# Performance work log

Hardware: AMD Instinct MI355X
Metric: run time of the kernel (lower is better)

## Reference

```python
import jax, jax.numpy as jnp
import numpy as np

N = 10000      # nodes
E = 80000      # edges
D = 128        # d_model
H = 8          # num_heads
DH = 128       # d_head
DFF = 512      # d_ff
CLAMP = 5.0
EPS = 1e-5


def setup_inputs() -> dict:
    key = jax.random.key(0)
    ks = jax.random.split(key, 10)
    s = 0.05
    return {
        "feat": jax.random.normal(ks[0], (N, D), jnp.float32),
        "src": jax.random.randint(ks[1], (E,), 0, N),
        "dst": jax.random.randint(ks[2], (E,), 0, N),
        # projections stored as (in, out); x @ W == torch Linear(bias=False)
        "Wq": jax.random.normal(ks[3], (D, H * DH), jnp.float32) * s,
        "Wk": jax.random.normal(ks[4], (D, H * DH), jnp.float32) * s,
        "Wv": jax.random.normal(ks[5], (D, H * DH), jnp.float32) * s,
        "Wo": jax.random.normal(ks[6], (H * DH, D), jnp.float32) * s,
        "g1": jnp.ones((D,), jnp.float32),
        "b1": jnp.zeros((D,), jnp.float32),
        "W1": jax.random.normal(ks[7], (D, DFF), jnp.float32) * s,
        "bf1": jnp.zeros((DFF,), jnp.float32),
        "W2": jax.random.normal(ks[8], (DFF, D), jnp.float32) * s,
        "bf2": jnp.zeros((D,), jnp.float32),
        "g2": jnp.ones((D,), jnp.float32),
        "b2": jnp.zeros((D,), jnp.float32),
    }


def _layer_norm(x, g, b):
    mu = x.mean(-1, keepdims=True)
    xc = x - mu
    var = (xc * xc).mean(-1, keepdims=True)
    return xc * jax.lax.rsqrt(var + EPS) * g + b


def reference(feat, src, dst, Wq, Wk, Wv, Wo, g1, b1, W1, bf1, W2, bf2, g2, b2):
    h_src = feat[src]                              # (E, D) gather
    h_dst = feat[dst]                              # (E, D)
    q = (h_dst @ Wq).reshape(E, H, DH)             # query from destination node
    k = (h_src @ Wk).reshape(E, H, DH)
    v = (h_src @ Wv).reshape(E, H, DH)
    # per-edge logits: QK dot per head, scale, clamp
    u = jnp.clip((q * k).sum(-1) / np.sqrt(DH), -CLAMP, CLAMP)  # (E, H)
    # edge_softmax over incoming edges of each destination node
    m = jax.ops.segment_max(u, dst, num_segments=N)             # (N, H)
    ex = jnp.exp(u - m[dst])
    den = jax.ops.segment_sum(ex, dst, num_segments=N)          # (N, H)
    a = ex / den[dst]                                           # (E, H)
    # weighted V, segment-sum to destination nodes
    agg = jax.ops.segment_sum(a[..., None] * v, dst, num_segments=N)  # (N, H, DH)
    uh = _layer_norm(feat + agg.reshape(N, H * DH) @ Wo, g1, b1)
    ffn = jax.nn.relu(uh @ W1 + bf1) @ W2 + bf2
    return _layer_norm(uh + ffn, g2, b2)
```

## Files before the change

### kernel.cpp

```cpp
#include <hip/hip_runtime.h>

typedef unsigned int uint;
typedef unsigned short ushort;
typedef __attribute__((ext_vector_type(8))) short short8;
typedef __attribute__((ext_vector_type(4))) float f32x4;

#define DEV static __device__ __forceinline__

DEV float bf_lo(uint v) { return __uint_as_float(v << 16); }
DEV float bf_hi(uint v) { return __uint_as_float(v & 0xffff0000u); }
DEV ushort f2bf(float f) {
    uint u = __float_as_uint(f);
    u += 0x7fffu + ((u >> 16) & 1u);
    return (ushort)(u >> 16);
}
DEV void stC(float* p, float v) { *p = v; }
DEV void stC(ushort* p, float v) { *p = f2bf(v); }

#define DPPADD(v, ctrl) \
    ((v) + __int_as_float(__builtin_amdgcn_mov_dpp(__float_as_int(v), (ctrl), 0xF, 0xF, true)))

template <typename OT>
DEV void transp_body(float (*tile)[65], const float* __restrict__ in,
                     OT* __restrict__ out, int R, int C, int bid, int t)
{
    const int nbx = C >> 6;
    const int bx = bid % nbx, by = bid / nbx;
#pragma unroll
    for (int it = 0; it < 4; ++it) {
        int idx = it * 256 + t;
        int rr = idx >> 4, cc4 = (idx & 15) * 4;
        float4 v = *reinterpret_cast<const float4*>(in + (size_t)(by * 64 + rr) * C + bx * 64 + cc4);
        tile[cc4][rr] = v.x; tile[cc4 + 1][rr] = v.y;
        tile[cc4 + 2][rr] = v.z; tile[cc4 + 3][rr] = v.w;
    }
    __syncthreads();
#pragma unroll
    for (int it = 0; it < 4; ++it) {
        int idx = it * 256 + t;
        int cc = idx >> 4, rr4 = (idx & 15) * 4;
        OT* po = out + (size_t)(bx * 64 + cc) * R + by * 64 + rr4;
        if constexpr (__is_same(OT, float)) {
            float4 o = { tile[cc][rr4], tile[cc][rr4 + 1], tile[cc][rr4 + 2], tile[cc][rr4 + 3] };
            *reinterpret_cast<float4*>(po) = o;
        } else {
            ushort4 o = { f2bf(tile[cc][rr4]), f2bf(tile[cc][rr4 + 1]),
                          f2bf(tile[cc][rr4 + 2]), f2bf(tile[cc][rr4 + 3]) };
            *reinterpret_cast<ushort4*>(po) = o;
        }
    }
}

__global__ __launch_bounds__(256) void prep1_kernel(
    int4* __restrict__ cntd4, int nz,
    const float* __restrict__ feat, ushort* __restrict__ featbf,
    const float* __restrict__ Wo, float* __restrict__ WoT,
    const float* __restrict__ W1, ushort* __restrict__ W1T,
    const float* __restrict__ W2, ushort* __restrict__ W2T, int N)
{
    __shared__ float tile[64][65];
    const int zb = (nz + 255) / 256;
    const int nf = (N * 32 + 255) / 256;
    const int b = blockIdx.x, t = threadIdx.x;
    if (b < zb) {
        int i = b * 256 + t;
        if (i < nz) cntd4[i] = int4{0, 0, 0, 0};
    } else if (b < zb + nf) {
        int i = (b - zb) * 256 + t;
        if (i >= N * 32) return;
        float4 v = reinterpret_cast<const float4*>(feat)[i];
        ushort4 o;
        o.x = f2bf(v.x); o.y = f2bf(v.y); o.z = f2bf(v.z); o.w = f2bf(v.w);
        reinterpret_cast<ushort4*>(featbf)[i] = o;
    } else if (b < zb + nf + 32) {
        transp_body<float>(tile, Wo, WoT, 1024, 128, b - zb - nf, t);
    } else if (b < zb + nf + 48) {
        transp_body<ushort>(tile, W1, W1T, 128, 512, b - zb - nf - 32, t);
    } else {
        transp_body<ushort>(tile, W2, W2T, 512, 128, b - zb - nf - 48, t);
    }
}

__global__ __launch_bounds__(256) void hist_mpt_kernel(
    const int* __restrict__ dst, int* __restrict__ cntd, int E, int eb,
    const float* __restrict__ Wq, const float* __restrict__ Wk,
    const float* __restrict__ Wv, const float* __restrict__ WoT,
    ushort* __restrict__ MPT)
{
    __shared__ char lds[65536];
    const int b = blockIdx.x, t = threadIdx.x;
    if (b < eb) {
        int e = b * 256 + t;
        if (e < E) atomicAdd(&cntd[dst[e]], 1);
        return;
    }
    char* As = lds;
    char* Bs = lds + 32768;

    const int mb = b - eb;
    const int part = mb >> 3, h = mb & 7;
    const int lane = t & 63, w = t >> 6;
    const int frow = lane & 15, kgrp = lane >> 4;

    const float* Asrc = part ? WoT : Wk;
    const float* Bsrc = part ? Wv : Wq;
    const float ascale = part ? 1.f : 0.08838834764831845f;

#pragma unroll
    for (int it = 0; it < 16; ++it) {
        int idx = it * 256 + t;
        int r = idx >> 5, c4 = (idx & 31) * 4;
        size_t goff = (size_t)r * 1024 + h * 128 + c4;
        float4 va = *reinterpret_cast<const float4*>(Asrc + goff);
        ushort4 ua = { f2bf(va.x * ascale), f2bf(va.y * ascale),
                       f2bf(va.z * ascale), f2bf(va.w * ascale) };
        *reinterpret_cast<ushort4*>(&As[r * 256 + ((c4 * 2) ^ ((r & 7) << 4))]) = ua;
        float4 vb = *reinterpret_cast<const float4*>(Bsrc + goff);
        ushort4 ub = { f2bf(vb.x), f2bf(vb.y), f2bf(vb.z), f2bf(vb.w) };
        *reinterpret_cast<ushort4*>(&Bs[r * 256 + ((c4 * 2) ^ ((r & 7) << 4))]) = ub;
    }
    __syncthreads();

    f32x4 acc[2][8] = {};
#pragma unroll
    for (int ks = 0; ks < 4; ++ks) {
        int koff = ks * 64 + kgrp * 16;
        short8 bfr[8];
#pragma unroll
        for (int fn = 0; fn < 8; ++fn) {
            int col = fn * 16 + frow;
            bfr[fn] = *reinterpret_cast<const short8*>(&Bs[col * 256 + (koff ^ ((col & 7) << 4))]);
        }
#pragma unroll
        for (int fm = 0; fm < 2; ++fm) {
            int row = w * 32 + fm * 16 + frow;
            short8 a = *reinterpret_cast<const short8*>(&As[row * 256 + (koff ^ ((row & 7) << 4))]);
#pragma unroll
            for (int fn = 0; fn < 8; ++fn)
                acc[fm][fn] = __builtin_amdgcn_mfma_f32_16x16x32_bf16(a, bfr[fn], acc[fm][fn], 0, 0, 0);
        }
    }

    const size_t base = ((size_t)part * 1024 + h * 128) * 128;
#pragma unroll
    for (int fm = 0; fm < 2; ++fm)
#pragma unroll
        for (int fn = 0; fn < 8; ++fn)
#pragma unroll
            for (int r = 0; r < 4; ++r) {
                int j = w * 32 + fm * 16 + kgrp * 4 + r;
                int i = fn * 16 + frow;
                MPT[base + (size_t)j * 128 + i] = f2bf(acc[fm][fn][r]);
            }
}

__global__ __launch_bounds__(1024) void scan1_kernel(
    const int* __restrict__ cntd, int* __restrict__ offd, int* __restrict__ curd, int N)
{
    __shared__ int ls[1024];
    const int t = threadIdx.x;
    const int chunk = (N + 1023) >> 10;
    int base = t * chunk;
    int s = 0;
    for (int i = 0; i < chunk; ++i) {
        int idx = base + i;
        if (idx < N) s += cntd[idx];
    }
    ls[t] = s;
    __syncthreads();
    for (int d = 1; d < 1024; d <<= 1) {
        int v = (t >= d) ? ls[t - d] : 0;
        __syncthreads();
        ls[t] += v;
        __syncthreads();
    }
    int run = t ? ls[t - 1] : 0;
    for (int i = 0; i < chunk; ++i) {
        int idx = base + i;
        if (idx < N) {
            offd[idx] = run;
            curd[idx] = run;
            run += cntd[idx];
        }
    }
    if (t == 1023) offd[N] = run;
}

__global__ __launch_bounds__(256) void gvo_scat_kernel(
    const ushort* __restrict__ A, const ushort* __restrict__ BT,
    ushort* __restrict__ C, int M, int nbg,
    const int* __restrict__ src, const int* __restrict__ dst,
    int* __restrict__ curd, int* __restrict__ src_d, int* __restrict__ dst_d, int E)
{
    __shared__ char lds[32768];
    const int b = blockIdx.x, t = threadIdx.x;

    if (b >= nbg) {
        int e = (b - nbg) * 256 + t;
        if (e >= E) return;
        int s = src[e], d = dst[e];
        int pd = atomicAdd(&curd[d], 1);
        src_d[pd] = s;
        dst_d[pd] = d;
        return;
    }

    char* AsB = lds;
    char* BsB = lds + 16384;
    const int m0 = (b >> 4) * 128;
    const int n0 = (b & 15) * 128;
    const int lane = t & 63, wid = t >> 6;
    const int wm = wid >> 1, wn = wid & 1;
    const int frow = lane & 15, kgrp = lane >> 4;

    f32x4 acc[4][4] = {};

    for (int kk = 0; kk < 128; kk += 64) {
#pragma unroll
        for (int it = 0; it < 4; ++it) {
            int q = it * 256 + t;
            int r = q >> 3, c8 = (q & 7) * 8;
            int gm = m0 + r;
            short8 v = {};
            if (gm < M) v = *reinterpret_cast<const short8*>(&A[(size_t)gm * 128 + kk + c8]);
            *reinterpret_cast<short8*>(&AsB[r * 128 + ((c8 * 2) ^ ((r & 7) << 4))]) = v;
        }
#pragma unroll
        for (int it = 0; it < 4; ++it) {
            int q = it * 256 + t;
            int r = q >> 3, c8 = (q & 7) * 8;
            short8 v = *reinterpret_cast<const short8*>(&BT[(size_t)(n0 + r) * 128 + kk + c8]);
            *reinterpret_cast<short8*>(&BsB[r * 128 + ((c8 * 2) ^ ((r & 7) << 4))]) = v;
        }
        __syncthreads();
#pragma unroll
        for (int kp = 0; kp < 2; ++kp) {
            const int koffb = kp * 64 + kgrp * 16;
            short8 bb[4];
#pragma unroll
            for (int fn = 0; fn < 4; ++fn) {
                int col = wn * 64 + fn * 16 + frow;
                bb[fn] = *reinterpret_cast<const short8*>(&BsB[col * 128 + (koffb ^ ((col & 7) << 4))]);
            }
#pragma unroll
            for (int fm = 0; fm < 4; ++fm) {
                int row = wm * 64 + fm * 16 + frow;
                short8 a = *reinterpret_cast<const short8*>(&AsB[row * 128 + (koffb ^ ((row & 7) << 4))]);
#pragma unroll
                for (int fn = 0; fn < 4; ++fn)
                    acc[fm][fn] = __builtin_amdgcn_mfma_f32_16x16x32_bf16(a, bb[fn], acc[fm][fn], 0, 0, 0);
            }
        }
        __syncthreads();
    }

#pragma unroll
    for (int fm = 0; fm < 4; ++fm)
#pragma unroll
        for (int fn = 0; fn < 4; ++fn)
#pragma unroll
            for (int r = 0; r < 4; ++r) {
                int gm = m0 + wm * 64 + fm * 16 + kgrp * 4 + r;
                int gn = n0 + wn * 64 + fn * 16 + frow;
                if (gm >= M) continue;
                stC(&C[(size_t)gm * 2048 + gn], acc[fm][fn][r]);
            }
}

__global__ __launch_bounds__(256) void edge_fused_kernel(
    const ushort* __restrict__ featbf, const ushort* __restrict__ GVO,
    const int* __restrict__ src_d, const int* __restrict__ dst_d,
    const int* __restrict__ offd, float* __restrict__ exws,
    const float* __restrict__ feat, const float* __restrict__ g1,
    const float* __restrict__ b1, float* __restrict__ uh,
    ushort* __restrict__ uhbf, int N)
{
    const int d0 = blockIdx.x * 4;
    const int t = threadIdx.x;
    const int blo = offd[d0];
    const int bhi = offd[min(d0 + 4, N)];

    {
        int g = t >> 4, li = t & 15;
        for (int p = blo + g; p < bhi; p += 16) {
            int s = src_d[p], d = dst_d[p];
            uint4 f = reinterpret_cast<const uint4*>(featbf)[(size_t)s * 16 + li];
            const uint4* Grow = reinterpret_cast<const uint4*>(GVO) + (size_t)d * 256 + li;
            float sel = 0.f;
#pragma unroll
            for (int h = 0; h < 8; ++h) {
                uint4 gv = Grow[h * 16];
                float pv = bf_lo(gv.x) * bf_lo(f.x) + bf_hi(gv.x) * bf_hi(f.x);
                pv += bf_lo(gv.y) * bf_lo(f.y) + bf_hi(gv.y) * bf_hi(f.y);
                pv += bf_lo(gv.z) * bf_lo(f.z) + bf_hi(gv.z) * bf_hi(f.z);
                pv += bf_lo(gv.w) * bf_lo(f.w) + bf_hi(gv.w) * bf_hi(f.w);
                pv = DPPADD(pv, 0xB1);
                pv = DPPADD(pv, 0x4E);
                pv = DPPADD(pv, 0x141);
                pv = DPPADD(pv, 0x128);
                sel = (li == h) ? pv : sel;
            }
            float u = fminf(fmaxf(sel, -5.f), 5.f);
            float ex = __expf(u);
            if (li < 8) exws[(size_t)p * 8 + li] = ex;
        }
    }
    __threadfence_block();
    __syncthreads();

    const int lane = t & 63;
    const int d = d0 + (t >> 6);
    if (d >= N) return;
    const int lo = offd[d], hi = offd[d + 1];

    int h = lane & 7;
    float den = 0.f;
    for (int i = lo + (lane >> 3); i < hi; i += 8)
        den += exws[(size_t)i * 8 + h];
    den += __shfl_xor(den, 8);
    den += __shfl_xor(den, 16);
    den += __shfl_xor(den, 32);
    float rh = 1.f / den;
    float rv0 = __shfl(rh, 0), rv1 = __shfl(rh, 1), rv2 = __shfl(rh, 2), rv3 = __shfl(rh, 3);
    float rv4 = __shfl(rh, 4), rv5 = __shfl(rh, 5), rv6 = __shfl(rh, 6), rv7 = __shfl(rh, 7);

    float acc0 = 0.f, acc1 = 0.f;
    int snext = (lo < hi) ? src_d[lo] : 0;
    for (int i = lo; i < hi; ++i) {
        int s = snext;
        if (i + 1 < hi) snext = src_d[i + 1];
        float4 e0 = *reinterpret_cast<const float4*>(&exws[(size_t)i * 8]);
        float4 e1 = *reinterpret_cast<const float4*>(&exws[(size_t)i * 8 + 4]);
        const uint* vrow = reinterpret_cast<const uint*>(GVO + (size_t)s * 2048 + 1024);
        uint gv0 = vrow[0 * 64 + lane], gv1 = vrow[1 * 64 + lane];
        uint gv2 = vrow[2 * 64 + lane], gv3 = vrow[3 * 64 + lane];
        uint gv4 = vrow[4 * 64 + lane], gv5 = vrow[5 * 64 + lane];
        uint gv6 = vrow[6 * 64 + lane], gv7 = vrow[7 * 64 + lane];
        float a0 = e0.x * rv0, a1 = e0.y * rv1, a2 = e0.z * rv2, a3 = e0.w * rv3;
        float a4 = e1.x * rv4, a5 = e1.y * rv5, a6 = e1.z * rv6, a7 = e1.w * rv7;
        acc0 += a0 * bf_lo(gv0) + a1 * bf_lo(gv1) + a2 * bf_lo(gv2) + a3 * bf_lo(gv3)
              + a4 * bf_lo(gv4) + a5 * bf_lo(gv5) + a6 * bf_lo(gv6) + a7 * bf_lo(gv7);
        acc1 += a0 * bf_hi(gv0) + a1 * bf_hi(gv1) + a2 * bf_hi(gv2) + a3 * bf_hi(gv3)
              + a4 * bf_hi(gv4) + a5 * bf_hi(gv5) + a6 * bf_hi(gv6) + a7 * bf_hi(gv7);
    }

    float2 v = reinterpret_cast<const float2*>(feat)[(size_t)d * 64 + lane];
    v.x += acc0;
    v.y += acc1;
    float sum = v.x + v.y;
#pragma unroll
    for (int off = 32; off; off >>= 1) sum += __shfl_xor(sum, off);
    float mean = sum * (1.f / 128.f);
    float cx = v.x - mean, cy = v.y - mean;
    float vs = cx * cx + cy * cy;
#pragma unroll
    for (int off = 32; off; off >>= 1) vs += __shfl_xor(vs, off);
    float r = rsqrtf(vs * (1.f / 128.f) + 1e-5f);
    float2 gg = reinterpret_cast<const float2*>(g1)[lane];
    float2 bb = reinterpret_cast<const float2*>(b1)[lane];
    float2 o;
    o.x = cx * r * gg.x + bb.x;
    o.y = cy * r * gg.y + bb.y;
    reinterpret_cast<float2*>(uh)[(size_t)d * 64 + lane] = o;
    ushort2 ob; ob.x = f2bf(o.x); ob.y = f2bf(o.y);
    reinterpret_cast<ushort2*>(uhbf)[(size_t)d * 64 + lane] = ob;
}

template <int NTILE, typename OT, bool BIAS, bool RELU, bool RES>
__global__ __launch_bounds__(256) void gemm_mfma(
    const ushort* __restrict__ A, const ushort* __restrict__ BT,
    const float* __restrict__ bias, const float* __restrict__ res,
    OT* __restrict__ C, int M, int K, int NC)
{
    constexpr int FN = NTILE * 2;
    constexpr int WN = NTILE * 32;
    __shared__ char lds[16384 + NTILE * 8192];
    char* AsB = lds;
    char* BsB = lds + 16384;

    const int m0 = blockIdx.y * 128;
    const int n0 = blockIdx.x * (NTILE * 64);
    const int t = threadIdx.x;
    const int lane = t & 63, wid = t >> 6;
    const int wm = wid >> 1, wn = wid & 1;
    const int frow = lane & 15, kgrp = lane >> 4;

    f32x4 acc[4][FN] = {};

    for (int kk = 0; kk < K; kk += 64) {
#pragma unroll
        for (int it = 0; it < 4; ++it) {
            int q = it * 256 + t;
            int r = q >> 3, c8 = (q & 7) * 8;
            int gm = m0 + r;
            short8 v = {};
            if (gm < M) v = *reinterpret_cast<const short8*>(&A[(size_t)gm * K + kk + c8]);
            *reinterpret_cast<short8*>(&AsB[r * 128 + ((c8 * 2) ^ ((r & 7) << 4))]) = v;
        }
#pragma unroll
        for (int it = 0; it < 2 * NTILE; ++it) {
            int q = it * 256 + t;
            int r = q >> 3, c8 = (q & 7) * 8;
            short8 v = *reinterpret_cast<const short8*>(&BT[(size_t)(n0 + r) * K + kk + c8]);
            *reinterpret_cast<short8*>(&BsB[r * 128 + ((c8 * 2) ^ ((r & 7) << 4))]) = v;
        }
        __syncthreads();
#pragma unroll
        for (int kp = 0; kp < 2; ++kp) {
            const int koffb = kp * 64 + kgrp * 16;
            short8 b[FN];
#pragma unroll
            for (int fn = 0; fn < FN; ++fn) {
                int col = wn * WN + fn * 16 + frow;
                b[fn] = *reinterpret_cast<const short8*>(&BsB[col * 128 + (koffb ^ ((col & 7) << 4))]);
            }
#pragma unroll
            for (int fm = 0; fm < 4; ++fm) {
                int row = wm * 64 + fm * 16 + frow;
                short8 a = *reinterpret_cast<const short8*>(&AsB[row * 128 + (koffb ^ ((row & 7) << 4))]);
#pragma unroll
                for (int fn = 0; fn < FN; ++fn)
                    acc[fm][fn] = __builtin_amdgcn_mfma_f32_16x16x32_bf16(a, b[fn], acc[fm][fn], 0, 0, 0);
            }
        }
        __syncthreads();
    }

#pragma unroll
    for (int fm = 0; fm < 4; ++fm)
#pragma unroll
        for (int fn = 0; fn < FN; ++fn)
#pragma unroll
            for (int r = 0; r < 4; ++r) {
                int gm = m0 + wm * 64 + fm * 16 + kgrp * 4 + r;
                int gn = n0 + wn * WN + fn * 16 + frow;
                if (gm >= M) continue;
                float v = acc[fm][fn][r];
                if (BIAS) v += bias[gn];
                if (RELU) v = fmaxf(v, 0.f);
                if (RES) v += res[(size_t)gm * NC + gn];
                stC(&C[(size_t)gm * NC + gn], v);
            }
}

__global__ __launch_bounds__(256) void gemm_mfma64(
    const ushort* __restrict__ A, const ushort* __restrict__ BT,
    const float* __restrict__ bias, const float* __restrict__ res,
    float* __restrict__ C, int M, int K, int NC)
{
    __shared__ char lds[16384];
    char* AsB = lds;
    char* BsB = lds + 8192;

    const int m0 = blockIdx.y * 64;
    const int n0 = blockIdx.x * 64;
    const int t = threadIdx.x;
    const int lane = t & 63, wid = t >> 6;
    const int wm = wid >> 1, wn = wid & 1;
    const int frow = lane & 15, kgrp = lane >> 4;

    f32x4 acc[2][2] = {};

    for (int kk = 0; kk < K; kk += 64) {
#pragma unroll
        for (int it = 0; it < 2; ++it) {
            int q = it * 256 + t;
            int r = q >> 3, c8 = (q & 7) * 8;
            int gm = m0 + r;
            short8 v = {};
            if (gm < M) v = *reinterpret_cast<const short8*>(&A[(size_t)gm * K + kk + c8]);
            *reinterpret_cast<short8*>(&AsB[r * 128 + ((c8 * 2) ^ ((r & 7) << 4))]) = v;
        }
#pragma unroll
        for (int it = 0; it < 2; ++it) {
            int q = it * 256 + t;
            int r = q >> 3, c8 = (q & 7) * 8;
            short8 v = *reinterpret_cast<const short8*>(&BT[(size_t)(n0 + r) * K + kk + c8]);
            *reinterpret_cast<short8*>(&BsB[r * 128 + ((c8 * 2) ^ ((r & 7) << 4))]) = v;
        }
        __syncthreads();
#pragma unroll
        for (int kp = 0; kp < 2; ++kp) {
            const int koffb = kp * 64 + kgrp * 16;
            short8 b[2];
#pragma unroll
            for (int fn = 0; fn < 2; ++fn) {
                int col = wn * 32 + fn * 16 + frow;
                b[fn] = *reinterpret_cast<const short8*>(&BsB[col * 128 + (koffb ^ ((col & 7) << 4))]);
            }
#pragma unroll
            for (int fm = 0; fm < 2; ++fm) {
                int row = wm * 32 + fm * 16 + frow;
                short8 a = *reinterpret_cast<const short8*>(&AsB[row * 128 + (koffb ^ ((row & 7) << 4))]);
#pragma unroll
                for (int fn = 0; fn < 2; ++fn)
                    acc[fm][fn] = __builtin_amdgcn_mfma_f32_16x16x32_bf16(a, b[fn], acc[fm][fn], 0, 0, 0);
            }
        }
        __syncthreads();
    }

#pragma unroll
    for (int fm = 0; fm < 2; ++fm)
#pragma unroll
        for (int fn = 0; fn < 2; ++fn)
#pragma unroll
            for (int r = 0; r < 4; ++r) {
                int gm = m0 + wm * 32 + fm * 16 + kgrp * 4 + r;
                int gn = n0 + wn * 32 + fn * 16 + frow;
                if (gm >= M) continue;
                float v = acc[fm][fn][r] + bias[gn] + res[(size_t)gm * NC + gn];
                C[(size_t)gm * NC + gn] = v;
            }
}

__global__ __launch_bounds__(256) void ln_kernel(
    const float* __restrict__ x, const float* __restrict__ g,
    const float* __restrict__ b, float* __restrict__ out, int M)
{
    int row = (int)((blockIdx.x * 256 + threadIdx.x) >> 6);
    int lane = threadIdx.x & 63;
    if (row >= M) return;
    float2 v = reinterpret_cast<const float2*>(x)[(size_t)row * 64 + lane];
    float sum = v.x + v.y;
#pragma unroll
    for (int off = 32; off; off >>= 1) sum += __shfl_xor(sum, off);
    float mean = sum * (1.f / 128.f);
    float cx = v.x - mean, cy = v.y - mean;
    float vs = cx * cx + cy * cy;
#pragma unroll
    for (int off = 32; off; off >>= 1) vs += __shfl_xor(vs, off);
    float r = rsqrtf(vs * (1.f / 128.f) + 1e-5f);
    float2 gg = reinterpret_cast<const float2*>(g)[lane];
    float2 bb = reinterpret_cast<const float2*>(b)[lane];
    float2 o;
    o.x = cx * r * gg.x + bb.x;
    o.y = cy * r * gg.y + bb.y;
    reinterpret_cast<float2*>(out)[(size_t)row * 64 + lane] = o;
}

extern "C" void kernel_launch(void* const* d_in, const int* in_sizes, int n_in,
                              void* d_out, int out_size, void* d_ws, size_t ws_size,
                              hipStream_t stream)
{
    const float* feat = (const float*)d_in[0];
    const int*   src  = (const int*)d_in[1];
    const int*   dst  = (const int*)d_in[2];
    const float* Wq   = (const float*)d_in[3];
    const float* Wk   = (const float*)d_in[4];
    const float* Wv   = (const float*)d_in[5];
    const float* Wo   = (const float*)d_in[6];
    const float* g1   = (const float*)d_in[7];
    const float* b1   = (const float*)d_in[8];
    const float* W1   = (const float*)d_in[9];
    const float* bf1  = (const float*)d_in[10];
    const float* W2   = (const float*)d_in[11];
    const float* bf2  = (const float*)d_in[12];
    const float* g2   = (const float*)d_in[13];
    const float* b2   = (const float*)d_in[14];
    const int N = in_sizes[0] / 128;
    const int E = in_sizes[1];
    float* out = (float*)d_out;

    char* w = (char*)d_ws;
    auto alloc = [&](size_t bytes) {
        char* p = w;
        w += (bytes + 255) & ~(size_t)255;
        return p;
    };
    ushort* MPT    = (ushort*)alloc((size_t)2048 * 128 * 2);
    float*  WoT    = (float*)alloc((size_t)128 * 1024 * 4);
    ushort* W1T    = (ushort*)alloc((size_t)512 * 128 * 2);
    ushort* W2T    = (ushort*)alloc((size_t)128 * 512 * 2);
    ushort* featbf = (ushort*)alloc((size_t)N * 128 * 2);
    ushort* GVO    = (ushort*)alloc((size_t)N * 2048 * 2);
    float*  exws   = (float*)alloc((size_t)E * 8 * 4);
    int*    cntd   = (int*)alloc((size_t)((N + 3) & ~3) * 4);
    int*    offd   = (int*)alloc((size_t)(N + 1) * 4);
    int*    curd   = (int*)alloc((size_t)N * 4);
    int*    src_d  = (int*)alloc((size_t)E * 4);
    int*    dst_d  = (int*)alloc((size_t)E * 4);
    float*  uh     = (float*)alloc((size_t)N * 128 * 4);
    ushort* uhbf   = (ushort*)alloc((size_t)N * 128 * 2);
    ushort* f1     = (ushort*)alloc((size_t)N * 512 * 2);
    float*  pre2   = (float*)alloc((size_t)N * 128 * 4);

    int nz = (N + 3) / 4;
    int zb = (nz + 255) / 256;
    int nf = (N * 32 + 255) / 256;
    prep1_kernel<<<zb + nf + 64, 256, 0, stream>>>(
        (int4*)cntd, nz, feat, featbf, Wo, WoT, W1, W1T, W2, W2T, N);

    int eb = (E + 255) / 256;
    hist_mpt_kernel<<<eb + 16, 256, 0, stream>>>(
        dst, cntd, E, eb, Wq, Wk, Wv, WoT, MPT);

    scan1_kernel<<<1, 1024, 0, stream>>>(cntd, offd, curd, N);

    int nbg = 16 * ((N + 127) / 128);
    gvo_scat_kernel<<<nbg + eb, 256, 0, stream>>>(
        featbf, MPT, GVO, N, nbg, src, dst, curd, src_d, dst_d, E);

    edge_fused_kernel<<<(N + 3) / 4, 256, 0, stream>>>(
        featbf, GVO, src_d, dst_d, offd, exws, feat, g1, b1, uh, uhbf, N);

    dim3 f1_grid(512 / 128, (N + 127) / 128);
    gemm_mfma<2, ushort, true, true, false><<<f1_grid, 256, 0, stream>>>(
        uhbf, W1T, bf1, nullptr, f1, N, 128, 512);
    dim3 f2_grid(128 / 64, (N + 63) / 64);
    gemm_mfma64<<<f2_grid, 256, 0, stream>>>(
        f1, W2T, bf2, uh, pre2, N, 512, 128);
    int nwaves_n = (N * 64 + 255) / 256;
    ln_kernel<<<nwaves_n, 256, 0, stream>>>(pre2, g2, b2, out, N);
}
```

Before: 122.9 us.

## Use direct global-to-LDS loads in GEMMs and prefetch next V row in aggregation

All MFMA GEMM tile loads now use the global_load_lds builtin with 16-byte transfers. This writes global data straight into LDS without staging through VGPRs, and the XOR swizzle moves onto the global address side. The edge aggregation loop now double-buffers by loading the next edge's V row and exp weights while it accumulates the current one, so gather latency is hidden. The GEMM change drops the `gm < M` row guard, so the last partial M tile may read past the end of A unless that buffer is padded.

```diff
diff --git a/kernel.cpp b/kernel.cpp
--- a/kernel.cpp
+++ b/kernel.cpp
@@ -19,6 +19,14 @@
 
 #define DPPADD(v, ctrl) \
     ((v) + __int_as_float(__builtin_amdgcn_mov_dpp(__float_as_int(v), (ctrl), 0xF, 0xF, true)))
+
+DEV void gload16(const void* gsrc, void* ldst)
+{
+    __builtin_amdgcn_global_load_lds(
+        (__attribute__((address_space(1))) void*)const_cast<void*>(gsrc),
+        (__attribute__((address_space(3))) void*)ldst,
+        16, 0, 0);
+}
 
 template <typename OT>
 DEV void transp_body(float (*tile)[65], const float* __restrict__ in,
@@ -212,6 +220,7 @@
     const int lane = t & 63, wid = t >> 6;
     const int wm = wid >> 1, wn = wid & 1;
     const int frow = lane & 15, kgrp = lane >> 4;
+    const int wub = (t & 192) * 16;
 
     f32x4 acc[4][4] = {};
 
@@ -219,18 +228,18 @@
 #pragma unroll
         for (int it = 0; it < 4; ++it) {
             int q = it * 256 + t;
-            int r = q >> 3, c8 = (q & 7) * 8;
-            int gm = m0 + r;
-            short8 v = {};
-            if (gm < M) v = *reinterpret_cast<const short8*>(&A[(size_t)gm * 128 + kk + c8]);
-            *reinterpret_cast<short8*>(&AsB[r * 128 + ((c8 * 2) ^ ((r & 7) << 4))]) = v;
+            int r = q >> 3;
+            int swz = ((q & 7) * 16) ^ ((r & 7) << 4);
+            gload16((const char*)A + ((size_t)(m0 + r) * 128 + kk) * 2 + swz,
+                    AsB + it * 4096 + wub);
         }
 #pragma unroll
         for (int it = 0; it < 4; ++it) {
             int q = it * 256 + t;
-            int r = q >> 3, c8 = (q & 7) * 8;
-            short8 v = *reinterpret_cast<const short8*>(&BT[(size_t)(n0 + r) * 128 + kk + c8]);
-            *reinterpret_cast<short8*>(&BsB[r * 128 + ((c8 * 2) ^ ((r & 7) << 4))]) = v;
+            int r = q >> 3;
+            int swz = ((q & 7) * 16) ^ ((r & 7) << 4);
+            gload16((const char*)BT + ((size_t)(n0 + r) * 128 + kk) * 2 + swz,
+                    BsB + it * 4096 + wub);
         }
         __syncthreads();
 #pragma unroll
@@ -325,23 +334,36 @@
     float rv4 = __shfl(rh, 4), rv5 = __shfl(rh, 5), rv6 = __shfl(rh, 6), rv7 = __shfl(rh, 7);
 
     float acc0 = 0.f, acc1 = 0.f;
-    int snext = (lo < hi) ? src_d[lo] : 0;
+    uint cg0 = 0, cg1 = 0, cg2 = 0, cg3 = 0, cg4 = 0, cg5 = 0, cg6 = 0, cg7 = 0;
+    float4 ce0 = {}, ce1 = {};
+    if (lo < hi) {
+        int s0 = src_d[lo];
+        const uint* vr = reinterpret_cast<const uint*>(GVO + (size_t)s0 * 2048 + 1024);
+        cg0 = vr[lane];       cg1 = vr[64 + lane];  cg2 = vr[128 + lane]; cg3 = vr[192 + lane];
+        cg4 = vr[256 + lane]; cg5 = vr[320 + lane]; cg6 = vr[384 + lane]; cg7 = vr[448 + lane];
+        ce0 = *reinterpret_cast<const float4*>(&exws[(size_t)lo * 8]);
+        ce1 = *reinterpret_cast<const float4*>(&exws[(size_t)lo * 8 + 4]);
+    }
     for (int i = lo; i < hi; ++i) {
-        int s = snext;
-        if (i + 1 < hi) snext = src_d[i + 1];
-        float4 e0 = *reinterpret_cast<const float4*>(&exws[(size_t)i * 8]);
-        float4 e1 = *reinterpret_cast<const float4*>(&exws[(size_t)i * 8 + 4]);
-        const uint* vrow = reinterpret_cast<const uint*>(GVO + (size_t)s * 2048 + 1024);
-        uint gv0 = vrow[0 * 64 + lane], gv1 = vrow[1 * 64 + lane];
-        uint gv2 = vrow[2 * 64 + lane], gv3 = vrow[3 * 64 + lane];
-        uint gv4 = vrow[4 * 64 + lane], gv5 = vrow[5 * 64 + lane];
-        uint gv6 = vrow[6 * 64 + lane], gv7 = vrow[7 * 64 + lane];
-        float a0 = e0.x * rv0, a1 = e0.y * rv1, a2 = e0.z * rv2, a3 = e0.w * rv3;
-        float a4 = e1.x * rv4, a5 = e1.y * rv5, a6 = e1.z * rv6, a7 = e1.w * rv7;
-        acc0 += a0 * bf_lo(gv0) + a1 * bf_lo(gv1) + a2 * bf_lo(gv2) + a3 * bf_lo(gv3)
-              + a4 * bf_lo(gv4) + a5 * bf_lo(gv5) + a6 * bf_lo(gv6) + a7 * bf_lo(gv7);
-        acc1 += a0 * bf_hi(gv0) + a1 * bf_hi(gv1) + a2 * bf_hi(gv2) + a3 * bf_hi(gv3)
-              + a4 * bf_hi(gv4) + a5 * bf_hi(gv5) + a6 * bf_hi(gv6) + a7 * bf_hi(gv7);
+        uint ng0 = 0, ng1 = 0, ng2 = 0, ng3 = 0, ng4 = 0, ng5 = 0, ng6 = 0, ng7 = 0;
+        float4 ne0 = {}, ne1 = {};
+        if (i + 1 < hi) {
+            int sn = src_d[i + 1];
+            const uint* vr = reinterpret_cast<const uint*>(GVO + (size_t)sn * 2048 + 1024);
+            ng0 = vr[lane];       ng1 = vr[64 + lane];  ng2 = vr[128 + lane]; ng3 = vr[192 + lane];
+            ng4 = vr[256 + lane]; ng5 = vr[320 + lane]; ng6 = vr[384 + lane]; ng7 = vr[448 + lane];
+            ne0 = *reinterpret_cast<const float4*>(&exws[(size_t)(i + 1) * 8]);
+            ne1 = *reinterpret_cast<const float4*>(&exws[(size_t)(i + 1) * 8 + 4]);
+        }
+        float a0 = ce0.x * rv0, a1 = ce0.y * rv1, a2 = ce0.z * rv2, a3 = ce0.w * rv3;
+        float a4 = ce1.x * rv4, a5 = ce1.y * rv5, a6 = ce1.z * rv6, a7 = ce1.w * rv7;
+        acc0 += a0 * bf_lo(cg0) + a1 * bf_lo(cg1) + a2 * bf_lo(cg2) + a3 * bf_lo(cg3)
+              + a4 * bf_lo(cg4) + a5 * bf_lo(cg5) + a6 * bf_lo(cg6) + a7 * bf_lo(cg7);
+        acc1 += a0 * bf_hi(cg0) + a1 * bf_hi(cg1) + a2 * bf_hi(cg2) + a3 * bf_hi(cg3)
+              + a4 * bf_hi(cg4) + a5 * bf_hi(cg5) + a6 * bf_hi(cg6) + a7 * bf_hi(cg7);
+        cg0 = ng0; cg1 = ng1; cg2 = ng2; cg3 = ng3;
+        cg4 = ng4; cg5 = ng5; cg6 = ng6; cg7 = ng7;
+        ce0 = ne0; ce1 = ne1;
     }
 
     float2 v = reinterpret_cast<const float2*>(feat)[(size_t)d * 64 + lane];
@@ -384,6 +406,7 @@
     const int lane = t & 63, wid = t >> 6;
     const int wm = wid >> 1, wn = wid & 1;
     const int frow = lane & 15, kgrp = lane >> 4;
+    const int wub = (t & 192) * 16;
 
     f32x4 acc[4][FN] = {};
 
@@ -391,18 +414,18 @@
 #pragma unroll
         for (int it = 0; it < 4; ++it) {
             int q = it * 256 + t;
-            int r = q >> 3, c8 = (q & 7) * 8;
-            int gm = m0 + r;
-            short8 v = {};
-            if (gm < M) v = *reinterpret_cast<const short8*>(&A[(size_t)gm * K + kk + c8]);
-            *reinterpret_cast<short8*>(&AsB[r * 128 + ((c8 * 2) ^ ((r & 7) << 4))]) = v;
+            int r = q >> 3;
+            int swz = ((q & 7) * 16) ^ ((r & 7) << 4);
+            gload16((const char*)A + ((size_t)(m0 + r) * K + kk) * 2 + swz,
+                    AsB + it * 4096 + wub);
         }
 #pragma unroll
         for (int it = 0; it < 2 * NTILE; ++it) {
             int q = it * 256 + t;
-            int r = q >> 3, c8 = (q & 7) * 8;
-            short8 v = *reinterpret_cast<const short8*>(&BT[(size_t)(n0 + r) * K + kk + c8]);
-            *reinterpret_cast<short8*>(&BsB[r * 128 + ((c8 * 2) ^ ((r & 7) << 4))]) = v;
+            int r = q >> 3;
+            int swz = ((q & 7) * 16) ^ ((r & 7) << 4);
+            gload16((const char*)BT + ((size_t)(n0 + r) * K + kk) * 2 + swz,
+                    BsB + it * 4096 + wub);
         }
         __syncthreads();
 #pragma unroll
@@ -458,6 +481,7 @@
     const int lane = t & 63, wid = t >> 6;
     const int wm = wid >> 1, wn = wid & 1;
     const int frow = lane & 15, kgrp = lane >> 4;
+    const int wub = (t & 192) * 16;
 
     f32x4 acc[2][2] = {};
 
@@ -465,18 +489,18 @@
 #pragma unroll
         for (int it = 0; it < 2; ++it) {
             int q = it * 256 + t;
-            int r = q >> 3, c8 = (q & 7) * 8;
-            int gm = m0 + r;
-            short8 v = {};
-            if (gm < M) v = *reinterpret_cast<const short8*>(&A[(size_t)gm * K + kk + c8]);
-            *reinterpret_cast<short8*>(&AsB[r * 128 + ((c8 * 2) ^ ((r & 7) << 4))]) = v;
+            int r = q >> 3;
+            int swz = ((q & 7) * 16) ^ ((r & 7) << 4);
+            gload16((const char*)A + ((size_t)(m0 + r) * K + kk) * 2 + swz,
+                    AsB + it * 4096 + wub);
         }
 #pragma unroll
         for (int it = 0; it < 2; ++it) {
             int q = it * 256 + t;
-            int r = q >> 3, c8 = (q & 7) * 8;
-            short8 v = *reinterpret_cast<const short8*>(&BT[(size_t)(n0 + r) * K + kk + c8]);
-            *reinterpret_cast<short8*>(&BsB[r * 128 + ((c8 * 2) ^ ((r & 7) << 4))]) = v;
+            int r = q >> 3;
+            int swz = ((q & 7) * 16) ^ ((r & 7) << 4);
+            gload16((const char*)BT + ((size_t)(n0 + r) * K + kk) * 2 + swz,
+                    BsB + it * 4096 + wub);
         }
         __syncthreads();
 #pragma unroll
```

Result: no change. 124.2 us (+1.0%).

## Fuse edge logits, softmax and aggregation per wave using MFMA scores

Applied to the files above, without the earlier changes.

Each wave now handles one destination node end to end. It computes the per-edge, per-head logits for 16 edges at a time with bf16 MFMA, using the node's precomputed query-projection rows as the A fragment and gathered source features as B. Exponentials are staged in LDS and accumulated directly into per-head V sums, and normalisation by the denominator is deferred to the end. This removes the exws global buffer, the dst_d array and the block-wide sync between the logit and aggregation phases. The cost is MFMA lanes wasted on partial 16-edge batches at low-degree nodes, plus extra LDS traffic per edge.

```diff
diff --git a/kernel.cpp b/kernel.cpp
--- a/kernel.cpp
+++ b/kernel.cpp
@@ -16,9 +16,6 @@
 }
 DEV void stC(float* p, float v) { *p = v; }
 DEV void stC(ushort* p, float v) { *p = f2bf(v); }
-
-#define DPPADD(v, ctrl) \
-    ((v) + __int_as_float(__builtin_amdgcn_mov_dpp(__float_as_int(v), (ctrl), 0xF, 0xF, true)))
 
 template <typename OT>
 DEV void transp_body(float (*tile)[65], const float* __restrict__ in,
@@ -190,7 +187,7 @@
     const ushort* __restrict__ A, const ushort* __restrict__ BT,
     ushort* __restrict__ C, int M, int nbg,
     const int* __restrict__ src, const int* __restrict__ dst,
-    int* __restrict__ curd, int* __restrict__ src_d, int* __restrict__ dst_d, int E)
+    int* __restrict__ curd, int* __restrict__ src_d, int E)
 {
     __shared__ char lds[32768];
     const int b = blockIdx.x, t = threadIdx.x;
@@ -201,7 +198,6 @@
         int s = src[e], d = dst[e];
         int pd = atomicAdd(&curd[d], 1);
         src_d[pd] = s;
-        dst_d[pd] = d;
         return;
     }
 
@@ -269,79 +265,89 @@
 
 __global__ __launch_bounds__(256) void edge_fused_kernel(
     const ushort* __restrict__ featbf, const ushort* __restrict__ GVO,
-    const int* __restrict__ src_d, const int* __restrict__ dst_d,
-    const int* __restrict__ offd, float* __restrict__ exws,
+    const int* __restrict__ src_d, const int* __restrict__ offd,
     const float* __restrict__ feat, const float* __restrict__ g1,
     const float* __restrict__ b1, float* __restrict__ uh,
     ushort* __restrict__ uhbf, int N)
 {
-    const int d0 = blockIdx.x * 4;
+    __shared__ float exl[4][16][8];
+    __shared__ int   srcl[4][16];
+
     const int t = threadIdx.x;
-    const int blo = offd[d0];
-    const int bhi = offd[min(d0 + 4, N)];
-
-    {
-        int g = t >> 4, li = t & 15;
-        for (int p = blo + g; p < bhi; p += 16) {
-            int s = src_d[p], d = dst_d[p];
-            uint4 f = reinterpret_cast<const uint4*>(featbf)[(size_t)s * 16 + li];
-            const uint4* Grow = reinterpret_cast<const uint4*>(GVO) + (size_t)d * 256 + li;
-            float sel = 0.f;
-#pragma unroll
-            for (int h = 0; h < 8; ++h) {
-                uint4 gv = Grow[h * 16];
-                float pv = bf_lo(gv.x) * bf_lo(f.x) + bf_hi(gv.x) * bf_hi(f.x);
-                pv += bf_lo(gv.y) * bf_lo(f.y) + bf_hi(gv.y) * bf_hi(f.y);
-                pv += bf_lo(gv.z) * bf_lo(f.z) + bf_hi(gv.z) * bf_hi(f.z);
-                pv += bf_lo(gv.w) * bf_lo(f.w) + bf_hi(gv.w) * bf_hi(f.w);
-                pv = DPPADD(pv, 0xB1);
-                pv = DPPADD(pv, 0x4E);
-                pv = DPPADD(pv, 0x141);
-                pv = DPPADD(pv, 0x128);
-                sel = (li == h) ? pv : sel;
-            }
-            float u = fminf(fmaxf(sel, -5.f), 5.f);
-            float ex = __expf(u);
-            if (li < 8) exws[(size_t)p * 8 + li] = ex;
-        }
-    }
-    __threadfence_block();
-    __syncthreads();
-
-    const int lane = t & 63;
-    const int d = d0 + (t >> 6);
+    const int lane = t & 63, wid = t >> 6;
+    const int frow = lane & 15, kgrp = lane >> 4;
+    const int d = blockIdx.x * 4 + wid;
     if (d >= N) return;
     const int lo = offd[d], hi = offd[d + 1];
-
-    int h = lane & 7;
-    float den = 0.f;
-    for (int i = lo + (lane >> 3); i < hi; i += 8)
-        den += exws[(size_t)i * 8 + h];
-    den += __shfl_xor(den, 8);
-    den += __shfl_xor(den, 16);
-    den += __shfl_xor(den, 32);
-    float rh = 1.f / den;
-    float rv0 = __shfl(rh, 0), rv1 = __shfl(rh, 1), rv2 = __shfl(rh, 2), rv3 = __shfl(rh, 3);
-    float rv4 = __shfl(rh, 4), rv5 = __shfl(rh, 5), rv6 = __shfl(rh, 6), rv7 = __shfl(rh, 7);
+    const int deg = hi - lo;
+
+    short8 afr[4];
+#pragma unroll
+    for (int ks = 0; ks < 4; ++ks)
+        afr[ks] = *reinterpret_cast<const short8*>(
+            &GVO[(size_t)d * 2048 + frow * 128 + ks * 32 + kgrp * 8]);
+
+    float acch0[8] = {}, acch1[8] = {};
+    float den_acc[4] = {};
+
+    for (int tb = 0; tb < deg; tb += 16) {
+        int ei = tb + frow;
+        int sv = (ei < deg) ? src_d[lo + ei] : 0;
+
+        f32x4 c = {};
+#pragma unroll
+        for (int ks = 0; ks < 4; ++ks) {
+            short8 bfr = *reinterpret_cast<const short8*>(
+                &featbf[(size_t)sv * 128 + ks * 32 + kgrp * 8]);
+            c = __builtin_amdgcn_mfma_f32_16x16x32_bf16(afr[ks], bfr, c, 0, 0, 0);
+        }
+
+        float exr[4];
+#pragma unroll
+        for (int r = 0; r < 4; ++r) {
+            float u = fminf(fmaxf(c[r], -5.f), 5.f);
+            exr[r] = __expf(u);
+        }
+        if (kgrp < 2)
+            *reinterpret_cast<float4*>(&exl[wid][frow][kgrp * 4]) =
+                float4{exr[0], exr[1], exr[2], exr[3]};
+        if (kgrp == 0) srcl[wid][frow] = sv;
+#pragma unroll
+        for (int r = 0; r < 4; ++r) {
+            float v = (ei < deg) ? exr[r] : 0.f;
+            v += __shfl_xor(v, 1); v += __shfl_xor(v, 2);
+            v += __shfl_xor(v, 4); v += __shfl_xor(v, 8);
+            den_acc[r] += v;
+        }
+
+        int vc = min(16, deg - tb);
+        for (int i = 0; i < vc; ++i) {
+            int s = srcl[wid][i];
+            float4 e0 = *reinterpret_cast<const float4*>(&exl[wid][i][0]);
+            float4 e1 = *reinterpret_cast<const float4*>(&exl[wid][i][4]);
+            const uint* vrow = reinterpret_cast<const uint*>(GVO + (size_t)s * 2048 + 1024);
+            uint gv0 = vrow[lane],       gv1 = vrow[64 + lane];
+            uint gv2 = vrow[128 + lane], gv3 = vrow[192 + lane];
+            uint gv4 = vrow[256 + lane], gv5 = vrow[320 + lane];
+            uint gv6 = vrow[384 + lane], gv7 = vrow[448 + lane];
+            acch0[0] += e0.x * bf_lo(gv0); acch1[0] += e0.x * bf_hi(gv0);
+            acch0[1] += e0.y * bf_lo(gv1); acch1[1] += e0.y * bf_hi(gv1);
+            acch0[2] += e0.z * bf_lo(gv2); acch1[2] += e0.z * bf_hi(gv2);
+            acch0[3] += e0.w * bf_lo(gv3); acch1[3] += e0.w * bf_hi(gv3);
+            acch0[4] += e1.x * bf_lo(gv4); acch1[4] += e1.x * bf_hi(gv4);
+            acch0[5] += e1.y * bf_lo(gv5); acch1[5] += e1.y * bf_hi(gv5);
+            acch0[6] += e1.z * bf_lo(gv6); acch1[6] += e1.z * bf_hi(gv6);
+            acch0[7] += e1.w * bf_lo(gv7); acch1[7] += e1.w * bf_hi(gv7);
+        }
+    }
 
     float acc0 = 0.f, acc1 = 0.f;
-    int snext = (lo < hi) ? src_d[lo] : 0;
-    for (int i = lo; i < hi; ++i) {
-        int s = snext;
-        if (i + 1 < hi) snext = src_d[i + 1];
-        float4 e0 = *reinterpret_cast<const float4*>(&exws[(size_t)i * 8]);
-        float4 e1 = *reinterpret_cast<const float4*>(&exws[(size_t)i * 8 + 4]);
-        const uint* vrow = reinterpret_cast<const uint*>(GVO + (size_t)s * 2048 + 1024);
-        uint gv0 = vrow[0 * 64 + lane], gv1 = vrow[1 * 64 + lane];
-        uint gv2 = vrow[2 * 64 + lane], gv3 = vrow[3 * 64 + lane];
-        uint gv4 = vrow[4 * 64 + lane], gv5 = vrow[5 * 64 + lane];
-        uint gv6 = vrow[6 * 64 + lane], gv7 = vrow[7 * 64 + lane];
-        float a0 = e0.x * rv0, a1 = e0.y * rv1, a2 = e0.z * rv2, a3 = e0.w * rv3;
-        float a4 = e1.x * rv4, a5 = e1.y * rv5, a6 = e1.z * rv6, a7 = e1.w * rv7;
-        acc0 += a0 * bf_lo(gv0) + a1 * bf_lo(gv1) + a2 * bf_lo(gv2) + a3 * bf_lo(gv3)
-              + a4 * bf_lo(gv4) + a5 * bf_lo(gv5) + a6 * bf_lo(gv6) + a7 * bf_lo(gv7);
-        acc1 += a0 * bf_hi(gv0) + a1 * bf_hi(gv1) + a2 * bf_hi(gv2) + a3 * bf_hi(gv3)
-              + a4 * bf_hi(gv4) + a5 * bf_hi(gv5) + a6 * bf_hi(gv6) + a7 * bf_hi(gv7);
+#pragma unroll
+    for (int h = 0; h < 8; ++h) {
+        float dh = __shfl(den_acc[h & 3], (h & 4) << 2);
+        float rd = (dh > 0.f) ? 1.f / dh : 0.f;
+        acc0 += acch0[h] * rd;
+        acc1 += acch1[h] * rd;
     }
 
     float2 v = reinterpret_cast<const float2*>(feat)[(size_t)d * 64 + lane];
@@ -574,12 +580,10 @@
     ushort* W2T    = (ushort*)alloc((size_t)128 * 512 * 2);
     ushort* featbf = (ushort*)alloc((size_t)N * 128 * 2);
     ushort* GVO    = (ushort*)alloc((size_t)N * 2048 * 2);
-    float*  exws   = (float*)alloc((size_t)E * 8 * 4);
     int*    cntd   = (int*)alloc((size_t)((N + 3) & ~3) * 4);
     int*    offd   = (int*)alloc((size_t)(N + 1) * 4);
     int*    curd   = (int*)alloc((size_t)N * 4);
     int*    src_d  = (int*)alloc((size_t)E * 4);
-    int*    dst_d  = (int*)alloc((size_t)E * 4);
     float*  uh     = (float*)alloc((size_t)N * 128 * 4);
     ushort* uhbf   = (ushort*)alloc((size_t)N * 128 * 2);
     ushort* f1     = (ushort*)alloc((size_t)N * 512 * 2);
@@ -599,10 +603,10 @@
 
     int nbg = 16 * ((N + 127) / 128);
     gvo_scat_kernel<<<nbg + eb, 256, 0, stream>>>(
-        featbf, MPT, GVO, N, nbg, src, dst, curd, src_d, dst_d, E);
+        featbf, MPT, GVO, N, nbg, src, dst, curd, src_d, E);
 
     edge_fused_kernel<<<(N + 3) / 4, 256, 0, stream>>>(
-        featbf, GVO, src_d, dst_d, offd, exws, feat, g1, b1, uh, uhbf, N);
+        featbf, GVO, src_d, offd, feat, g1, b1, uh, uhbf, N);
 
     dim3 f1_grid(512 / 128, (N + 127) / 128);
     gemm_mfma<2, ushort, true, true, false><<<f1_grid, 256, 0, stream>>>(
```

New measurement: 123.7 us. No clear change (+0.6%).
